# Kernel optimization log

Measured on AMD Instinct MI355X. Metric: run time of the kernel, lower is better.

## Reference

```python
import jax, jax.numpy as jnp
import numpy as np

NUM_EMB = 256
EMB_DIM = 128
COMMIT_COST = 0.25


def setup_inputs() -> dict:
    key = jax.random.key(0)
    k1, k2 = jax.random.split(key)
    z = jax.random.normal(k1, (64, EMB_DIM, 64, 64), dtype=jnp.float32)
    # codebook initialized uniform(-1/num_embeddings, 1/num_embeddings)
    emb = jax.random.uniform(k2, (NUM_EMB, EMB_DIM), dtype=jnp.float32,
                             minval=-1.0 / NUM_EMB, maxval=1.0 / NUM_EMB)
    return {"z": z, "emb": emb}


def reference(z, emb):
    B, C, H, W = z.shape
    # [B, C, H, W] -> [B*H*W, C]
    z_flat = jnp.transpose(z, (0, 2, 3, 1)).reshape(-1, C)
    # squared L2 distances to each code: ||z||^2 - 2 z.e + ||e||^2, shape [N, K]
    d = (jnp.sum(z_flat * z_flat, axis=1, keepdims=True)
         - 2.0 * jnp.einsum('nc,kc->nk', z_flat, emb)
         + jnp.sum(emb * emb, axis=1))
    idx = jnp.argmin(d, axis=1)  # [N]
    # gather codes, back to NCHW
    quantized = emb[idx].reshape(B, H, W, C)
    quantized = jnp.transpose(quantized, (0, 3, 1, 2))
    commitment_loss = COMMIT_COST * jnp.mean(
        (jax.lax.stop_gradient(quantized) - z) ** 2)
    codebook_loss = jnp.mean((quantized - jax.lax.stop_gradient(z)) ** 2)
    # straight-through estimator
    quantized_ste = z + jax.lax.stop_gradient(quantized - z)
    return (quantized_ste, idx.reshape(B, H, W), commitment_loss, codebook_loss)
```

## Files before the change

kernel.cpp:

```cpp
#include <hip/hip_runtime.h>

#define K_EMB   256
#define C_DIM   128
#define HW      4096
#define NPOS    262144
#define Q_ELEMS 33554432
#define IDX_OFF Q_ELEMS
#define LOSS_OFF (Q_ELEMS + NPOS)

#define BLKP 64
#define NTHR 512
#define NW   8
#define CC   16
#define NCHUNK (C_DIM / CC)
#define TM   4
#define TN   8
#define NG   32

#define WS_ENORM 0
#define WS_ACC   256
#define WS_EMBT  512
#define WS_NEED_FULL  ((WS_EMBT + C_DIM * K_EMB) * 4)

#define GLOAD16(gsrc, ldst) __builtin_amdgcn_global_load_lds(                 \
    (const __attribute__((address_space(1))) void*)(gsrc),                    \
    (__attribute__((address_space(3))) void*)(ldst), 16, 0, 0)

__global__ __launch_bounds__(K_EMB) void vq_prep(const float* __restrict__ emb,
                                                 float* __restrict__ ws,
                                                 int use_embT) {
    const int c = blockIdx.x, k = threadIdx.x;
    if (c < C_DIM) {
        if (use_embT) ws[WS_EMBT + c * K_EMB + k] = emb[k * C_DIM + c];
        if (c == 0 && k == 0) ws[WS_ACC] = 0.f;
    } else {
        const float4* __restrict__ er = reinterpret_cast<const float4*>(emb + k * C_DIM);
        float s = 0.f;
        #pragma unroll
        for (int j = 0; j < C_DIM / 4; ++j) {
            float4 v = er[j];
            s = fmaf(v.x, v.x, s);
            s = fmaf(v.y, v.y, s);
            s = fmaf(v.z, v.z, s);
            s = fmaf(v.w, v.w, s);
        }
        ws[WS_ENORM + k] = s;
    }
}

template <int UT>
__global__ __launch_bounds__(NTHR, 4) void vq_main(const float* __restrict__ z,
                                                   const float* __restrict__ emb,
                                                   const float* __restrict__ ws,
                                                   float* __restrict__ out,
                                                   float* __restrict__ loss_acc) {
    __shared__ float zlds[C_DIM * BLKP];
    __shared__ float ebuf[2][CC * K_EMB];
    __shared__ float shen[K_EMB];
    __shared__ float shpb[NG * BLKP];
    __shared__ unsigned int shpi[NG * BLKP / 4];

    const int t    = threadIdx.x;
    const int lane = t & 63;
    const int w    = t >> 6;
    const int pg   = lane & 15;
    const int cg   = lane >> 4;
    const int p0   = pg * 4;
    const int k0   = w * 32 + cg * 8;
    const int blk  = blockIdx.x;
    const int b    = blk >> 6;
    const int hw0  = (blk & 63) * BLKP;
    const size_t zoff = (size_t)b * (C_DIM * HW) + hw0;
    const float* __restrict__ zsrc = z + zoff;

    const float* __restrict__ embT    = ws + WS_EMBT;
    const float* __restrict__ enorm_g = ws + WS_ENORM;

    #pragma unroll
    for (int j = 0; j < 4; ++j) {
        const int i4 = t + j * NTHR;
        const int c  = i4 >> 4;
        const int p4 = i4 & 15;
        GLOAD16(zsrc + (size_t)c * HW + p4 * 4, &zlds[i4 * 4]);
    }
    if (UT) {
        #pragma unroll
        for (int s = 0; s < 2; ++s) {
            const int i4 = t + s * NTHR;
            GLOAD16(embT + i4 * 4, &ebuf[0][i4 * 4]);
        }
    }
    if (t < K_EMB) shen[t] = enorm_g[t];
    __syncthreads();

    float acc[TM][TN];
    float zn[TM];
    #pragma unroll
    for (int i = 0; i < TM; ++i) {
        zn[i] = 0.f;
        #pragma unroll
        for (int j = 0; j < TN; ++j) acc[i][j] = 0.f;
    }

    if (UT) {
        for (int ch = 0; ch < NCHUNK; ++ch) {
            if (ch + 1 < NCHUNK) {
                const float* __restrict__ src = embT + (ch + 1) * CC * K_EMB;
                #pragma unroll
                for (int s = 0; s < 2; ++s) {
                    const int i4 = t + s * NTHR;
                    GLOAD16(src + i4 * 4, &ebuf[(ch + 1) & 1][i4 * 4]);
                }
            }
            const float* __restrict__ eb = ebuf[ch & 1];
            const int cbase = ch * CC;
            #pragma unroll 4
            for (int c = 0; c < CC; ++c) {
                const float4 zv = *reinterpret_cast<const float4*>(
                    &zlds[(cbase + c) * BLKP + p0]);
                const float4 e0 = *reinterpret_cast<const float4*>(
                    &eb[c * K_EMB + k0]);
                const float4 e1 = *reinterpret_cast<const float4*>(
                    &eb[c * K_EMB + k0 + 4]);
                const float zz[TM] = {zv.x, zv.y, zv.z, zv.w};
                const float ee[TN] = {e0.x, e0.y, e0.z, e0.w,
                                      e1.x, e1.y, e1.z, e1.w};
                #pragma unroll
                for (int i = 0; i < TM; ++i) {
                    zn[i] = fmaf(zz[i], zz[i], zn[i]);
                    #pragma unroll
                    for (int j = 0; j < TN; ++j)
                        acc[i][j] = fmaf(zz[i], ee[j], acc[i][j]);
                }
            }
            if (ch + 1 < NCHUNK) {
                __syncthreads();
            }
        }
    } else {
        #pragma unroll 2
        for (int c = 0; c < C_DIM; ++c) {
            const float4 zv = *reinterpret_cast<const float4*>(&zlds[c * BLKP + p0]);
            const float zz[TM] = {zv.x, zv.y, zv.z, zv.w};
            float ee[TN];
            #pragma unroll
            for (int j = 0; j < TN; ++j) ee[j] = emb[(k0 + j) * C_DIM + c];
            #pragma unroll
            for (int i = 0; i < TM; ++i) {
                zn[i] = fmaf(zz[i], zz[i], zn[i]);
                #pragma unroll
                for (int j = 0; j < TN; ++j)
                    acc[i][j] = fmaf(zz[i], ee[j], acc[i][j]);
            }
        }
    }

    {
        float pb[TM];
        int   pi_[TM];
        #pragma unroll
        for (int i = 0; i < TM; ++i) {
            float best = 3.402823466e38f;
            int   bi = 0;
            #pragma unroll
            for (int j = 0; j < TN; ++j) {
                const float d = (zn[i] - 2.0f * acc[i][j]) + shen[k0 + j];
                if (d < best) { best = d; bi = k0 + j; }
            }
            pb[i] = best; pi_[i] = bi;
        }
        const int g = w * 4 + cg;
        *reinterpret_cast<float4*>(&shpb[g * BLKP + p0]) =
            make_float4(pb[0], pb[1], pb[2], pb[3]);
        shpi[g * 16 + pg] = (unsigned)(pi_[0] & 255)
                          | ((unsigned)(pi_[1] & 255) << 8)
                          | ((unsigned)(pi_[2] & 255) << 16)
                          | ((unsigned)(pi_[3] & 255) << 24);
    }
    __syncthreads();

    if (t < BLKP) {
        const int p = t;
        float bb = shpb[p];
        int   bi = (int)((shpi[p >> 2] >> ((p & 3) * 8)) & 255u);
        #pragma unroll 4
        for (int g = 1; g < NG; ++g) {
            const float bq = shpb[g * BLKP + p];
            if (bq < bb) {
                bb = bq;
                bi = (int)((shpi[g * 16 + (p >> 2)] >> ((p & 3) * 8)) & 255u);
            }
        }
        const int fin = bi;
        const int pos = blk * BLKP + p;
        __builtin_nontemporal_store((float)fin, &out[IDX_OFF + pos]);

        float lsum = 0.f;
        float* qp = out + zoff + p;
        const float4* __restrict__ er =
            reinterpret_cast<const float4*>(emb + fin * C_DIM);
        #pragma unroll 4
        for (int j = 0; j < C_DIM / 4; ++j) {
            const float4 ev = er[j];
            const int c0 = j * 4;
            const float z0 = zlds[(c0 + 0) * BLKP + p];
            const float z1 = zlds[(c0 + 1) * BLKP + p];
            const float z2 = zlds[(c0 + 2) * BLKP + p];
            const float z3 = zlds[(c0 + 3) * BLKP + p];
            const float d0 = ev.x - z0, d1 = ev.y - z1;
            const float d2 = ev.z - z2, d3 = ev.w - z3;
            lsum = fmaf(d0, d0, lsum);
            lsum = fmaf(d1, d1, lsum);
            lsum = fmaf(d2, d2, lsum);
            lsum = fmaf(d3, d3, lsum);
            __builtin_nontemporal_store(z0 + d0, &qp[(size_t)(c0 + 0) * HW]);
            __builtin_nontemporal_store(z1 + d1, &qp[(size_t)(c0 + 1) * HW]);
            __builtin_nontemporal_store(z2 + d2, &qp[(size_t)(c0 + 2) * HW]);
            __builtin_nontemporal_store(z3 + d3, &qp[(size_t)(c0 + 3) * HW]);
        }

        #pragma unroll
        for (int off = 32; off > 0; off >>= 1)
            lsum += __shfl_down(lsum, off, 64);
        if (p == 0) atomicAdd(loss_acc, lsum);
    }
}

__global__ void vq_finalize(const float* __restrict__ loss_acc,
                            float* __restrict__ out_losses) {
    float S = loss_acc[0];
    float mean = S / (float)Q_ELEMS;
    out_losses[0] = 0.25f * mean;
    out_losses[1] = mean;
}

extern "C" void kernel_launch(void* const* d_in, const int* in_sizes, int n_in,
                              void* d_out, int out_size, void* d_ws, size_t ws_size,
                              hipStream_t stream) {
    const float* z   = (const float*)d_in[0];
    const float* emb = (const float*)d_in[1];
    float* out = (float*)d_out;
    float* ws  = (float*)d_ws;

    int use_embT = (ws_size >= (size_t)WS_NEED_FULL) ? 1 : 0;

    vq_prep<<<C_DIM + 1, K_EMB, 0, stream>>>(emb, ws, use_embT);
    if (use_embT)
        vq_main<1><<<NPOS / BLKP, NTHR, 0, stream>>>(z, emb, ws, out, ws + WS_ACC);
    else
        vq_main<0><<<NPOS / BLKP, NTHR, 0, stream>>>(z, emb, ws, out, ws + WS_ACC);
    vq_finalize<<<1, 1, 0, stream>>>(ws + WS_ACC, out + LOSS_OFF);
}
```

Measured before the change: 412.2 us.

## Enlarge per-thread register tile to 8x8 and reduce argmin with wave shuffles

```diff
diff --git a/kernel.cpp b/kernel.cpp
--- a/kernel.cpp
+++ b/kernel.cpp
@@ -9,13 +9,12 @@
 #define LOSS_OFF (Q_ELEMS + NPOS)
 
 #define BLKP 64
-#define NTHR 512
-#define NW   8
-#define CC   16
+#define NTHR 256
+#define NW   4
+#define CC   8
 #define NCHUNK (C_DIM / CC)
-#define TM   4
+#define TM   8
 #define TN   8
-#define NG   32
 
 #define WS_ENORM 0
 #define WS_ACC   256
@@ -49,7 +48,7 @@
 }
 
 template <int UT>
-__global__ __launch_bounds__(NTHR, 4) void vq_main(const float* __restrict__ z,
+__global__ __launch_bounds__(NTHR, 3) void vq_main(const float* __restrict__ z,
                                                    const float* __restrict__ emb,
                                                    const float* __restrict__ ws,
                                                    float* __restrict__ out,
@@ -57,16 +56,16 @@
     __shared__ float zlds[C_DIM * BLKP];
     __shared__ float ebuf[2][CC * K_EMB];
     __shared__ float shen[K_EMB];
-    __shared__ float shpb[NG * BLKP];
-    __shared__ unsigned int shpi[NG * BLKP / 4];
+    __shared__ float shpb[NW * BLKP];
+    __shared__ int   shpi[NW * BLKP];
 
     const int t    = threadIdx.x;
     const int lane = t & 63;
     const int w    = t >> 6;
-    const int pg   = lane & 15;
-    const int cg   = lane >> 4;
-    const int p0   = pg * 4;
-    const int k0   = w * 32 + cg * 8;
+    const int cgl  = lane & 7;
+    const int pg   = lane >> 3;
+    const int p0   = pg * 8;
+    const int k0   = w * 64 + cgl * 8;
     const int blk  = blockIdx.x;
     const int b    = blk >> 6;
     const int hw0  = (blk & 63) * BLKP;
@@ -77,7 +76,7 @@
     const float* __restrict__ enorm_g = ws + WS_ENORM;
 
     #pragma unroll
-    for (int j = 0; j < 4; ++j) {
+    for (int j = 0; j < (C_DIM * BLKP / 4) / NTHR; ++j) {
         const int i4 = t + j * NTHR;
         const int c  = i4 >> 4;
         const int p4 = i4 & 15;
@@ -90,7 +89,7 @@
             GLOAD16(embT + i4 * 4, &ebuf[0][i4 * 4]);
         }
     }
-    if (t < K_EMB) shen[t] = enorm_g[t];
+    shen[t] = enorm_g[t];
     __syncthreads();
 
     float acc[TM][TN];
@@ -114,15 +113,18 @@
             }
             const float* __restrict__ eb = ebuf[ch & 1];
             const int cbase = ch * CC;
-            #pragma unroll 4
+            #pragma unroll
             for (int c = 0; c < CC; ++c) {
-                const float4 zv = *reinterpret_cast<const float4*>(
+                const float4 z0 = *reinterpret_cast<const float4*>(
                     &zlds[(cbase + c) * BLKP + p0]);
+                const float4 z1 = *reinterpret_cast<const float4*>(
+                    &zlds[(cbase + c) * BLKP + p0 + 4]);
                 const float4 e0 = *reinterpret_cast<const float4*>(
                     &eb[c * K_EMB + k0]);
                 const float4 e1 = *reinterpret_cast<const float4*>(
                     &eb[c * K_EMB + k0 + 4]);
-                const float zz[TM] = {zv.x, zv.y, zv.z, zv.w};
+                const float zz[TM] = {z0.x, z0.y, z0.z, z0.w,
+                                      z1.x, z1.y, z1.z, z1.w};
                 const float ee[TN] = {e0.x, e0.y, e0.z, e0.w,
                                       e1.x, e1.y, e1.z, e1.w};
                 #pragma unroll
@@ -140,8 +142,10 @@
     } else {
         #pragma unroll 2
         for (int c = 0; c < C_DIM; ++c) {
-            const float4 zv = *reinterpret_cast<const float4*>(&zlds[c * BLKP + p0]);
-            const float zz[TM] = {zv.x, zv.y, zv.z, zv.w};
+            const float4 z0 = *reinterpret_cast<const float4*>(&zlds[c * BLKP + p0]);
+            const float4 z1 = *reinterpret_cast<const float4*>(&zlds[c * BLKP + p0 + 4]);
+            const float zz[TM] = {z0.x, z0.y, z0.z, z0.w,
+                                  z1.x, z1.y, z1.z, z1.w};
             float ee[TN];
             #pragma unroll
             for (int j = 0; j < TN; ++j) ee[j] = emb[(k0 + j) * C_DIM + c];
@@ -155,43 +159,50 @@
         }
     }
 
-    {
-        float pb[TM];
-        int   pi_[TM];
+    float bb[TM];
+    int   bi[TM];
+    #pragma unroll
+    for (int i = 0; i < TM; ++i) {
+        float best = 3.402823466e38f;
+        int   bidx = 0;
+        #pragma unroll
+        for (int j = 0; j < TN; ++j) {
+            const float d = (zn[i] - 2.0f * acc[i][j]) + shen[k0 + j];
+            if (d < best) { best = d; bidx = k0 + j; }
+        }
+        bb[i] = best; bi[i] = bidx;
+    }
+
+    #pragma unroll
+    for (int m = 1; m <= 4; m <<= 1) {
         #pragma unroll
         for (int i = 0; i < TM; ++i) {
-            float best = 3.402823466e38f;
-            int   bi = 0;
-            #pragma unroll
-            for (int j = 0; j < TN; ++j) {
-                const float d = (zn[i] - 2.0f * acc[i][j]) + shen[k0 + j];
-                if (d < best) { best = d; bi = k0 + j; }
-            }
-            pb[i] = best; pi_[i] = bi;
-        }
-        const int g = w * 4 + cg;
-        *reinterpret_cast<float4*>(&shpb[g * BLKP + p0]) =
-            make_float4(pb[0], pb[1], pb[2], pb[3]);
-        shpi[g * 16 + pg] = (unsigned)(pi_[0] & 255)
-                          | ((unsigned)(pi_[1] & 255) << 8)
-                          | ((unsigned)(pi_[2] & 255) << 16)
-                          | ((unsigned)(pi_[3] & 255) << 24);
+            const float od = __shfl_xor(bb[i], m, 64);
+            const int   ok = __shfl_xor(bi[i], m, 64);
+            if (od < bb[i] || (od == bb[i] && ok < bi[i])) {
+                bb[i] = od; bi[i] = ok;
+            }
+        }
+    }
+    if (cgl == 0) {
+        #pragma unroll
+        for (int i = 0; i < TM; ++i) {
+            shpb[w * BLKP + p0 + i] = bb[i];
+            shpi[w * BLKP + p0 + i] = bi[i];
+        }
     }
     __syncthreads();
 
     if (t < BLKP) {
         const int p = t;
-        float bb = shpb[p];
-        int   bi = (int)((shpi[p >> 2] >> ((p & 3) * 8)) & 255u);
-        #pragma unroll 4
-        for (int g = 1; g < NG; ++g) {
-            const float bq = shpb[g * BLKP + p];
-            if (bq < bb) {
-                bb = bq;
-                bi = (int)((shpi[g * 16 + (p >> 2)] >> ((p & 3) * 8)) & 255u);
-            }
-        }
-        const int fin = bi;
+        float fb = shpb[p];
+        int   fi = shpi[p];
+        #pragma unroll
+        for (int w2 = 1; w2 < NW; ++w2) {
+            const float d = shpb[w2 * BLKP + p];
+            if (d < fb) { fb = d; fi = shpi[w2 * BLKP + p]; }
+        }
+        const int fin = fi;
         const int pos = blk * BLKP + p;
         __builtin_nontemporal_store((float)fin, &out[IDX_OFF + pos]);
 
@@ -203,20 +214,20 @@
         for (int j = 0; j < C_DIM / 4; ++j) {
             const float4 ev = er[j];
             const int c0 = j * 4;
-            const float z0 = zlds[(c0 + 0) * BLKP + p];
-            const float z1 = zlds[(c0 + 1) * BLKP + p];
-            const float z2 = zlds[(c0 + 2) * BLKP + p];
-            const float z3 = zlds[(c0 + 3) * BLKP + p];
-            const float d0 = ev.x - z0, d1 = ev.y - z1;
-            const float d2 = ev.z - z2, d3 = ev.w - z3;
+            const float y0 = zlds[(c0 + 0) * BLKP + p];
+            const float y1 = zlds[(c0 + 1) * BLKP + p];
+            const float y2 = zlds[(c0 + 2) * BLKP + p];
+            const float y3 = zlds[(c0 + 3) * BLKP + p];
+            const float d0 = ev.x - y0, d1 = ev.y - y1;
+            const float d2 = ev.z - y2, d3 = ev.w - y3;
             lsum = fmaf(d0, d0, lsum);
             lsum = fmaf(d1, d1, lsum);
             lsum = fmaf(d2, d2, lsum);
             lsum = fmaf(d3, d3, lsum);
-            __builtin_nontemporal_store(z0 + d0, &qp[(size_t)(c0 + 0) * HW]);
-            __builtin_nontemporal_store(z1 + d1, &qp[(size_t)(c0 + 1) * HW]);
-            __builtin_nontemporal_store(z2 + d2, &qp[(size_t)(c0 + 2) * HW]);
-            __builtin_nontemporal_store(z3 + d3, &qp[(size_t)(c0 + 3) * HW]);
+            __builtin_nontemporal_store(y0 + d0, &qp[(size_t)(c0 + 0) * HW]);
+            __builtin_nontemporal_store(y1 + d1, &qp[(size_t)(c0 + 1) * HW]);
+            __builtin_nontemporal_store(y2 + d2, &qp[(size_t)(c0 + 2) * HW]);
+            __builtin_nontemporal_store(y3 + d3, &qp[(size_t)(c0 + 3) * HW]);
         }
 
         #pragma unroll
```

Result: slower. 914.7 us (+121.9%).
